# Performance work log

Hardware: AMD Instinct MI355X
Metric: run time of the kernel (lower is better)

The kernel has to match this reference:

```python
import jax, jax.numpy as jnp
from jax import lax
import numpy as np

B, S, H, V = 128, 512, 1024, 128


def setup_inputs() -> dict:
    key = jax.random.key(0)
    ks = jax.random.split(key, 8)
    s = 1.0 / np.sqrt(H)
    return {
        "x": jax.random.randint(ks[0], (B, S), 0, V, dtype=jnp.int32),
        "emb": jax.random.normal(ks[1], (V, H), dtype=jnp.float32),
        "W_ih": jax.random.uniform(ks[2], (H, H), jnp.float32, -s, s),
        "W_hh": jax.random.uniform(ks[3], (H, H), jnp.float32, -s, s),
        "b_ih": jax.random.uniform(ks[4], (H,), jnp.float32, -s, s),
        "b_hh": jax.random.uniform(ks[5], (H,), jnp.float32, -s, s),
        "W_fc": jax.random.uniform(ks[6], (V, H), jnp.float32, -s, s),
        "b_fc": jax.random.uniform(ks[7], (V,), jnp.float32, -s, s),
    }


def reference(x, emb, W_ih, W_hh, b_ih, b_hh, W_fc, b_fc):
    # Embedding lookup: [B, S, H]
    xe = emb[x]
    # Batched input projection for all timesteps (one big GEMM), fold in both biases
    xp = jnp.einsum("bsh,ih->bsi", xe, W_ih) + (b_ih + b_hh)  # [B, S, H]
    h0 = jnp.zeros((x.shape[0], W_hh.shape[0]), dtype=xp.dtype)

    def step(h, xt):  # xt: [B, H]
        h_new = jnp.tanh(xt + h @ W_hh.T)
        return h_new, None

    hT, _ = lax.scan(step, h0, jnp.swapaxes(xp, 0, 1))  # scan over time
    # Final-step linear: [B, V]
    return hT @ W_fc.T + b_fc
```

## Files before the change

kernel.cpp:

```cpp
#include <hip/hip_runtime.h>
#include <hip/hip_bf16.h>
#include <stdint.h>

#define Bb 128
#define Ss 512
#define Hh 1024
#define Vv 128

#define GROUPS 8
#define WPG 16
#define MB 16
#define NCOL 64

typedef __attribute__((ext_vector_type(8))) short short8;
typedef __attribute__((ext_vector_type(4))) float float4v;
typedef __attribute__((ext_vector_type(4))) unsigned int uint4v;

static __device__ __forceinline__ short f2bf(float f) {
    union { float f; uint32_t u; } x; x.f = f;
    uint32_t r = x.u + 0x7FFFu + ((x.u >> 16) & 1u);
    return (short)(r >> 16);
}
static __device__ __forceinline__ float bf2f(uint16_t b) {
    union { uint32_t u; float f; } x; x.u = ((uint32_t)b) << 16;
    return x.f;
}
static __device__ __forceinline__ float ftanh(float x) {
    float e = __builtin_amdgcn_exp2f(x * 2.885390082f);
    return 1.0f - 2.0f * __builtin_amdgcn_rcpf(e + 1.0f);
}

__global__ void k_prep(const float* __restrict__ emb, const float* __restrict__ Wih,
                       const float* __restrict__ bih, const float* __restrict__ bhh,
                       float* __restrict__ P) {
    int v = blockIdx.x >> 2;
    int i = ((blockIdx.x & 3) << 8) + threadIdx.x;
    const float4v* e4 = (const float4v*)(emb + v * Hh);
    const float4v* w4 = (const float4v*)(Wih + i * Hh);
    float acc = 0.f;
    #pragma unroll 4
    for (int h = 0; h < Hh / 4; ++h) {
        float4v a = e4[h], b = w4[h];
        acc += a[0]*b[0] + a[1]*b[1] + a[2]*b[2] + a[3]*b[3];
    }
    P[v * Hh + i] = acc + bih[i] + bhh[i];
}

__launch_bounds__(256, 1)
__global__ void k_rnn(const int* __restrict__ x, const float* __restrict__ Whh,
                      const float* __restrict__ P,
                      uint32_t* __restrict__ h0u, uint32_t* __restrict__ h1u) {
    __shared__ int     x_lds[Ss][MB];
    __shared__ float   P_lds[Vv][NCOL];
    __shared__ float4v red[2][4][4][64];

    const int g    = blockIdx.x >> 4;
    const int w    = blockIdx.x & 15;
    const int r0   = g * MB;
    const int n0   = w * NCOL;
    const int tid  = threadIdx.x;
    const int lane = tid & 63;
    const int q    = tid >> 6;

    for (int l = tid; l < Ss * MB; l += 256) {
        int t = l >> 4, r = l & 15;
        x_lds[t][r] = x[(r0 + r) * Ss + t];
    }
    for (int l = tid; l < Vv * NCOL; l += 256) {
        int v = l >> 6, c = l & 63;
        P_lds[v][c] = P[v * Hh + n0 + c];
    }

    short8 bf[4][8];
    {
        const int n_lane = lane & 15;
        const int k_base = q * 256 + ((lane >> 4) << 3);
        #pragma unroll
        for (int nt = 0; nt < 4; ++nt) {
            const float* wrow = Whh + (size_t)(n0 + nt * 16 + n_lane) * Hh;
            #pragma unroll
            for (int s = 0; s < 8; ++s) {
                const float* src = wrow + k_base + s * 32;
                short8 tmp;
                #pragma unroll
                for (int e = 0; e < 8; ++e) tmp[e] = f2bf(src[e]);
                bf[nt][s] = tmp;
            }
        }
    }
    __syncthreads();

    const int row_base = (lane >> 4) << 2;
    const int c_lane   = lane & 15;
    int budget = 1 << 22;

    const int probe_off = (Hh * (r0 + 15)) + ((q << 2) + ((lane & 15) >> 2)) * 64
                          + ((lane & 3) << 4);

    for (int t = 0; t < Ss; ++t) {
        float4v acc0 = {0.f,0.f,0.f,0.f}, acc1 = {0.f,0.f,0.f,0.f};
        float4v acc2 = {0.f,0.f,0.f,0.f}, acc3 = {0.f,0.f,0.f,0.f};

        if (t > 0) {
            const uint32_t tag = (uint32_t)t;
            const uint32_t* hin = (t & 1) ? h1u : h0u;

            {
                const uint32_t* pp = hin + probe_off;
                for (;;) {
                    uint32_t fv;
                    asm volatile("global_load_dword %0, %1, off sc0 sc1\n\t"
                                 "s_waitcnt vmcnt(0)"
                                 : "=v"(fv) : "v"(pp) : "memory");
                    if (__all((int)((fv & 0xFFFFu) == tag))) break;
                    if (--budget <= 0) break;
                }
            }

            const uint32_t* arow = hin + (size_t)(r0 + c_lane) * Hh + q * 256
                                   + ((lane >> 4) << 3);
            uint4v dd[16];
            for (;;) {
                asm volatile(
                    "global_load_dwordx4 %0, %8, off sc0 sc1\n\t"
                    "global_load_dwordx4 %1, %8, off offset:16 sc0 sc1\n\t"
                    "global_load_dwordx4 %2, %8, off offset:128 sc0 sc1\n\t"
                    "global_load_dwordx4 %3, %8, off offset:144 sc0 sc1\n\t"
                    "global_load_dwordx4 %4, %8, off offset:256 sc0 sc1\n\t"
                    "global_load_dwordx4 %5, %8, off offset:272 sc0 sc1\n\t"
                    "global_load_dwordx4 %6, %8, off offset:384 sc0 sc1\n\t"
                    "global_load_dwordx4 %7, %8, off offset:400 sc0 sc1"
                    : "=&v"(dd[0]), "=&v"(dd[1]), "=&v"(dd[2]), "=&v"(dd[3]),
                      "=&v"(dd[4]), "=&v"(dd[5]), "=&v"(dd[6]), "=&v"(dd[7])
                    : "v"(arow) : "memory");
                asm volatile(
                    "global_load_dwordx4 %0, %8, off offset:512 sc0 sc1\n\t"
                    "global_load_dwordx4 %1, %8, off offset:528 sc0 sc1\n\t"
                    "global_load_dwordx4 %2, %8, off offset:640 sc0 sc1\n\t"
                    "global_load_dwordx4 %3, %8, off offset:656 sc0 sc1\n\t"
                    "global_load_dwordx4 %4, %8, off offset:768 sc0 sc1\n\t"
                    "global_load_dwordx4 %5, %8, off offset:784 sc0 sc1\n\t"
                    "global_load_dwordx4 %6, %8, off offset:896 sc0 sc1\n\t"
                    "global_load_dwordx4 %7, %8, off offset:912 sc0 sc1\n\t"
                    "s_waitcnt vmcnt(0)"
                    : "=&v"(dd[8]), "=&v"(dd[9]), "=&v"(dd[10]), "=&v"(dd[11]),
                      "=&v"(dd[12]), "=&v"(dd[13]), "=&v"(dd[14]), "=&v"(dd[15])
                    : "v"(arow) : "memory");
                uint32_t ok = 1u;
                #pragma unroll
                for (int i = 0; i < 16; ++i) ok &= (uint32_t)((dd[i].x & 0xFFFFu) == tag);
                if (__all((int)ok)) break;
                if (--budget <= 0) break;
            }

            #define PK(d0, d1) (((d0) >> 16) | ((d1) & 0xFFFF0000u))
            #pragma unroll
            for (int s = 0; s < 8; ++s) {
                uint4v lo = dd[2 * s], hi = dd[2 * s + 1];
                uint4v pk = { PK(lo.x, lo.y), PK(lo.z, lo.w),
                              PK(hi.x, hi.y), PK(hi.z, hi.w) };
                short8 a;
                __builtin_memcpy(&a, &pk, 16);
                acc0 = __builtin_amdgcn_mfma_f32_16x16x32_bf16(a, bf[0][s], acc0, 0,0,0);
                acc1 = __builtin_amdgcn_mfma_f32_16x16x32_bf16(a, bf[1][s], acc1, 0,0,0);
                acc2 = __builtin_amdgcn_mfma_f32_16x16x32_bf16(a, bf[2][s], acc2, 0,0,0);
                acc3 = __builtin_amdgcn_mfma_f32_16x16x32_bf16(a, bf[3][s], acc3, 0,0,0);
            }
            #undef PK
        }

        const int pb = t & 1;
        red[pb][q][0][lane] = acc0;
        red[pb][q][1][lane] = acc1;
        red[pb][q][2][lane] = acc2;
        red[pb][q][3][lane] = acc3;
        __syncthreads();

        {
            float4v u = red[pb][0][q][lane];
            u += red[pb][1][q][lane];
            u += red[pb][2][q][lane];
            u += red[pb][3][q][lane];
            uint32_t* hout = ((t + 1) & 1) ? h1u : h0u;
            const int pcol = q * 16 + c_lane;
            const int ncol = n0 + pcol;
            int v0i = x_lds[t][row_base + 0], v1i = x_lds[t][row_base + 1];
            int v2i = x_lds[t][row_base + 2], v3i = x_lds[t][row_base + 3];
            const uint32_t t1 = (uint32_t)(t + 1);
            uint32_t b0 = ((uint32_t)(uint16_t)f2bf(ftanh(u[0] + P_lds[v0i][pcol])) << 16) | t1;
            uint32_t b1 = ((uint32_t)(uint16_t)f2bf(ftanh(u[1] + P_lds[v1i][pcol])) << 16) | t1;
            uint32_t b2 = ((uint32_t)(uint16_t)f2bf(ftanh(u[2] + P_lds[v2i][pcol])) << 16) | t1;
            uint32_t b3 = ((uint32_t)(uint16_t)f2bf(ftanh(u[3] + P_lds[v3i][pcol])) << 16) | t1;
            uint32_t* p0 = hout + (size_t)(r0 + row_base) * Hh + ncol;
            asm volatile("global_store_dword %0, %1, off sc0 sc1"
                         :: "v"(p0),            "v"(b0) : "memory");
            asm volatile("global_store_dword %0, %1, off sc0 sc1"
                         :: "v"(p0 + Hh),       "v"(b1) : "memory");
            asm volatile("global_store_dword %0, %1, off sc0 sc1"
                         :: "v"(p0 + 2 * Hh),   "v"(b2) : "memory");
            asm volatile("global_store_dword %0, %1, off sc0 sc1"
                         :: "v"(p0 + 3 * Hh),   "v"(b3) : "memory");
        }
    }
}

__global__ void k_fc(const uint32_t* __restrict__ hT, const float* __restrict__ Wfc,
                     const float* __restrict__ bfc, float* __restrict__ out) {
    int bb = (blockIdx.x >> 3) << 4;
    int vb = (blockIdx.x & 7) << 4;
    int b  = bb + (threadIdx.x >> 4);
    int v  = vb + (threadIdx.x & 15);
    const uint32_t* hrow = hT + (size_t)b * Hh;
    const float*    wrow = Wfc + (size_t)v * Hh;
    float acc = 0.f;
    #pragma unroll 4
    for (int i = 0; i < Hh; i += 4) {
        float4v wv = *(const float4v*)(wrow + i);
        acc += bf2f((uint16_t)(hrow[i + 0] >> 16)) * wv[0]
             + bf2f((uint16_t)(hrow[i + 1] >> 16)) * wv[1]
             + bf2f((uint16_t)(hrow[i + 2] >> 16)) * wv[2]
             + bf2f((uint16_t)(hrow[i + 3] >> 16)) * wv[3];
    }
    out[(size_t)b * Vv + v] = acc + bfc[v];
}

extern "C" void kernel_launch(void* const* d_in, const int* in_sizes, int n_in,
                              void* d_out, int out_size, void* d_ws, size_t ws_size,
                              hipStream_t stream) {
    const int*   x   = (const int*)d_in[0];
    const float* emb = (const float*)d_in[1];
    const float* Wih = (const float*)d_in[2];
    const float* Whh = (const float*)d_in[3];
    const float* bih = (const float*)d_in[4];
    const float* bhh = (const float*)d_in[5];
    const float* Wfc = (const float*)d_in[6];
    const float* bfc = (const float*)d_in[7];
    float* out = (float*)d_out;

    char* ws = (char*)d_ws;
    float*    P   = (float*)ws;
    uint32_t* h0u = (uint32_t*)(ws + (512 << 10));
    uint32_t* h1u = (uint32_t*)(ws + (1024 << 10));

    k_prep<<<512, 256, 0, stream>>>(emb, Wih, bih, bhh, P);
    k_rnn<<<128, 256, 0, stream>>>(x, Whh, P, h0u, h1u);
    k_fc<<<64, 256, 0, stream>>>(h0u, Wfc, bfc, out);
}
```

Measured before the change: 1.908 ms.

## Halve RNN workgroups with wider column tiles and sleep-backoff polling

Each workgroup now owns 128 hidden columns instead of 64, so the persistent recurrent kernel runs on 64 blocks instead of 128. Each block holds twice as many W_hh fragments in registers and issues eight MFMA chains per k-step. The separate single-dword probe spin is removed and replaced by s_sleep backoff before and between full tag-checked loads. Token ids are stored in LDS as bytes to offset the larger P tile. The intent is to cut cross-block synchronization traffic and polling contention, at the cost of more per-block work per step and higher register pressure.

New measurement: 2.241 ms. 17.5% more time.

```diff
diff --git a/kernel.cpp b/kernel.cpp
--- a/kernel.cpp
+++ b/kernel.cpp
@@ -8,9 +8,9 @@
 #define Vv 128
 
 #define GROUPS 8
-#define WPG 16
+#define WPG 8
 #define MB 16
-#define NCOL 64
+#define NCOL 128
 
 typedef __attribute__((ext_vector_type(8))) short short8;
 typedef __attribute__((ext_vector_type(4))) float float4v;
@@ -50,12 +50,12 @@
 __global__ void k_rnn(const int* __restrict__ x, const float* __restrict__ Whh,
                       const float* __restrict__ P,
                       uint32_t* __restrict__ h0u, uint32_t* __restrict__ h1u) {
-    __shared__ int     x_lds[Ss][MB];
+    __shared__ uint8_t x_lds[Ss][MB];
     __shared__ float   P_lds[Vv][NCOL];
-    __shared__ float4v red[2][4][4][64];
-
-    const int g    = blockIdx.x >> 4;
-    const int w    = blockIdx.x & 15;
+    __shared__ float4v red[2][4][8][64];
+
+    const int g    = blockIdx.x >> 3;
+    const int w    = blockIdx.x & 7;
     const int r0   = g * MB;
     const int n0   = w * NCOL;
     const int tid  = threadIdx.x;
@@ -64,19 +64,19 @@
 
     for (int l = tid; l < Ss * MB; l += 256) {
         int t = l >> 4, r = l & 15;
-        x_lds[t][r] = x[(r0 + r) * Ss + t];
+        x_lds[t][r] = (uint8_t)x[(r0 + r) * Ss + t];
     }
     for (int l = tid; l < Vv * NCOL; l += 256) {
-        int v = l >> 6, c = l & 63;
+        int v = l >> 7, c = l & 127;
         P_lds[v][c] = P[v * Hh + n0 + c];
     }
 
-    short8 bf[4][8];
+    short8 bf[8][8];
     {
         const int n_lane = lane & 15;
         const int k_base = q * 256 + ((lane >> 4) << 3);
         #pragma unroll
-        for (int nt = 0; nt < 4; ++nt) {
+        for (int nt = 0; nt < 8; ++nt) {
             const float* wrow = Whh + (size_t)(n0 + nt * 16 + n_lane) * Hh;
             #pragma unroll
             for (int s = 0; s < 8; ++s) {
@@ -94,32 +94,19 @@
     const int c_lane   = lane & 15;
     int budget = 1 << 22;
 
-    const int probe_off = (Hh * (r0 + 15)) + ((q << 2) + ((lane & 15) >> 2)) * 64
-                          + ((lane & 3) << 4);
-
     for (int t = 0; t < Ss; ++t) {
         float4v acc0 = {0.f,0.f,0.f,0.f}, acc1 = {0.f,0.f,0.f,0.f};
         float4v acc2 = {0.f,0.f,0.f,0.f}, acc3 = {0.f,0.f,0.f,0.f};
+        float4v acc4 = {0.f,0.f,0.f,0.f}, acc5 = {0.f,0.f,0.f,0.f};
+        float4v acc6 = {0.f,0.f,0.f,0.f}, acc7 = {0.f,0.f,0.f,0.f};
 
         if (t > 0) {
             const uint32_t tag = (uint32_t)t;
             const uint32_t* hin = (t & 1) ? h1u : h0u;
-
-            {
-                const uint32_t* pp = hin + probe_off;
-                for (;;) {
-                    uint32_t fv;
-                    asm volatile("global_load_dword %0, %1, off sc0 sc1\n\t"
-                                 "s_waitcnt vmcnt(0)"
-                                 : "=v"(fv) : "v"(pp) : "memory");
-                    if (__all((int)((fv & 0xFFFFu) == tag))) break;
-                    if (--budget <= 0) break;
-                }
-            }
-
             const uint32_t* arow = hin + (size_t)(r0 + c_lane) * Hh + q * 256
                                    + ((lane >> 4) << 3);
             uint4v dd[16];
+            __builtin_amdgcn_s_sleep(16);
             for (;;) {
                 asm volatile(
                     "global_load_dwordx4 %0, %8, off sc0 sc1\n\t"
@@ -151,6 +138,7 @@
                 for (int i = 0; i < 16; ++i) ok &= (uint32_t)((dd[i].x & 0xFFFFu) == tag);
                 if (__all((int)ok)) break;
                 if (--budget <= 0) break;
+                __builtin_amdgcn_s_sleep(4);
             }
 
             #define PK(d0, d1) (((d0) >> 16) | ((d1) & 0xFFFF0000u))
@@ -165,6 +153,10 @@
                 acc1 = __builtin_amdgcn_mfma_f32_16x16x32_bf16(a, bf[1][s], acc1, 0,0,0);
                 acc2 = __builtin_amdgcn_mfma_f32_16x16x32_bf16(a, bf[2][s], acc2, 0,0,0);
                 acc3 = __builtin_amdgcn_mfma_f32_16x16x32_bf16(a, bf[3][s], acc3, 0,0,0);
+                acc4 = __builtin_amdgcn_mfma_f32_16x16x32_bf16(a, bf[4][s], acc4, 0,0,0);
+                acc5 = __builtin_amdgcn_mfma_f32_16x16x32_bf16(a, bf[5][s], acc5, 0,0,0);
+                acc6 = __builtin_amdgcn_mfma_f32_16x16x32_bf16(a, bf[6][s], acc6, 0,0,0);
+                acc7 = __builtin_amdgcn_mfma_f32_16x16x32_bf16(a, bf[7][s], acc7, 0,0,0);
             }
             #undef PK
         }
@@ -174,32 +166,40 @@
         red[pb][q][1][lane] = acc1;
         red[pb][q][2][lane] = acc2;
         red[pb][q][3][lane] = acc3;
+        red[pb][q][4][lane] = acc4;
+        red[pb][q][5][lane] = acc5;
+        red[pb][q][6][lane] = acc6;
+        red[pb][q][7][lane] = acc7;
         __syncthreads();
 
         {
-            float4v u = red[pb][0][q][lane];
-            u += red[pb][1][q][lane];
-            u += red[pb][2][q][lane];
-            u += red[pb][3][q][lane];
             uint32_t* hout = ((t + 1) & 1) ? h1u : h0u;
-            const int pcol = q * 16 + c_lane;
-            const int ncol = n0 + pcol;
+            const uint32_t t1 = (uint32_t)(t + 1);
             int v0i = x_lds[t][row_base + 0], v1i = x_lds[t][row_base + 1];
             int v2i = x_lds[t][row_base + 2], v3i = x_lds[t][row_base + 3];
-            const uint32_t t1 = (uint32_t)(t + 1);
-            uint32_t b0 = ((uint32_t)(uint16_t)f2bf(ftanh(u[0] + P_lds[v0i][pcol])) << 16) | t1;
-            uint32_t b1 = ((uint32_t)(uint16_t)f2bf(ftanh(u[1] + P_lds[v1i][pcol])) << 16) | t1;
-            uint32_t b2 = ((uint32_t)(uint16_t)f2bf(ftanh(u[2] + P_lds[v2i][pcol])) << 16) | t1;
-            uint32_t b3 = ((uint32_t)(uint16_t)f2bf(ftanh(u[3] + P_lds[v3i][pcol])) << 16) | t1;
-            uint32_t* p0 = hout + (size_t)(r0 + row_base) * Hh + ncol;
-            asm volatile("global_store_dword %0, %1, off sc0 sc1"
-                         :: "v"(p0),            "v"(b0) : "memory");
-            asm volatile("global_store_dword %0, %1, off sc0 sc1"
-                         :: "v"(p0 + Hh),       "v"(b1) : "memory");
-            asm volatile("global_store_dword %0, %1, off sc0 sc1"
-                         :: "v"(p0 + 2 * Hh),   "v"(b2) : "memory");
-            asm volatile("global_store_dword %0, %1, off sc0 sc1"
-                         :: "v"(p0 + 3 * Hh),   "v"(b3) : "memory");
+            #pragma unroll
+            for (int j = 0; j < 2; ++j) {
+                const int nt = (q << 1) + j;
+                float4v u = red[pb][0][nt][lane];
+                u += red[pb][1][nt][lane];
+                u += red[pb][2][nt][lane];
+                u += red[pb][3][nt][lane];
+                const int pcol = (nt << 4) + c_lane;
+                const int ncol = n0 + pcol;
+                uint32_t b0 = ((uint32_t)(uint16_t)f2bf(ftanh(u[0] + P_lds[v0i][pcol])) << 16) | t1;
+                uint32_t b1 = ((uint32_t)(uint16_t)f2bf(ftanh(u[1] + P_lds[v1i][pcol])) << 16) | t1;
+                uint32_t b2 = ((uint32_t)(uint16_t)f2bf(ftanh(u[2] + P_lds[v2i][pcol])) << 16) | t1;
+                uint32_t b3 = ((uint32_t)(uint16_t)f2bf(ftanh(u[3] + P_lds[v3i][pcol])) << 16) | t1;
+                uint32_t* p0 = hout + (size_t)(r0 + row_base) * Hh + ncol;
+                asm volatile("global_store_dword %0, %1, off sc0 sc1"
+                             :: "v"(p0),          "v"(b0) : "memory");
+                asm volatile("global_store_dword %0, %1, off sc0 sc1"
+                             :: "v"(p0 + Hh),     "v"(b1) : "memory");
+                asm volatile("global_store_dword %0, %1, off sc0 sc1"
+                             :: "v"(p0 + 2 * Hh), "v"(b2) : "memory");
+                asm volatile("global_store_dword %0, %1, off sc0 sc1"
+                             :: "v"(p0 + 3 * Hh), "v"(b3) : "memory");
+            }
         }
     }
 }
@@ -243,6 +243,6 @@
     uint32_t* h1u = (uint32_t*)(ws + (1024 << 10));
 
     k_prep<<<512, 256, 0, stream>>>(emb, Wih, bih, bhh, P);
-    k_rnn<<<128, 256, 0, stream>>>(x, Whh, P, h0u, h1u);
+    k_rnn<<<64, 256, 0, stream>>>(x, Whh, P, h0u, h1u);
     k_fc<<<64, 256, 0, stream>>>(h0u, Wfc, bfc, out);
 }
```
